# Optimization experiments

Hardware: AMD Instinct MI355X
Metric: run time of the kernel (lower is better)

Reference implementation:

```python
import jax, jax.numpy as jnp
import numpy as np
from functools import partial

NUM_ITERS = 3
NUM_CAPS = 8      # primary capsule count
NUM_CLASSES = 10
OUT_CH = 16       # digit capsule dim
INPUT_SIZE = 32 * 6 * 6  # 1152 primary capsule units per capsule map


def squash(s, axis=-1):
    # faithful to non_linear_squashing: s * (||s||^2/(1+||s||^2)) / (||s||+1e-10)
    norm_sqr = jnp.sum(s * s, axis=axis, keepdims=True)
    scale = jnp.sqrt(norm_sqr) + 1e-10
    mag = norm_sqr / (1.0 + norm_sqr)
    return s * mag / scale


def conv2d(x, w, b, stride):
    y = jax.lax.conv_general_dilated(
        x, w, window_strides=(stride, stride), padding='VALID',
        dimension_numbers=('NCHW', 'OIHW', 'NCHW'))
    return y + b[None, :, None, None]


def setup_inputs() -> dict:
    key = jax.random.key(0)
    ks = jax.random.split(key, 6)
    B = 256
    x = jax.random.normal(ks[0], (B, 1, 28, 28), dtype=jnp.float32)
    conv_w = jax.random.normal(ks[1], (256, 1, 9, 9), dtype=jnp.float32) * 0.05
    conv_b = jax.random.normal(ks[2], (256,), dtype=jnp.float32) * 0.05
    # 8 primary capsule conv units (256->32 each) fused into one 256->256 conv
    prim_w = jax.random.normal(ks[3], (NUM_CAPS * 32, 256, 9, 9), dtype=jnp.float32) * 0.02
    prim_b = jax.random.normal(ks[4], (NUM_CAPS * 32,), dtype=jnp.float32) * 0.02
    # digit routing weights (input_size, num_classes, out_channels, num_capsules)
    digit_w = jax.random.normal(ks[5], (INPUT_SIZE, NUM_CLASSES, OUT_CH, NUM_CAPS), dtype=jnp.float32)
    return {'x': x, 'conv_w': conv_w, 'conv_b': conv_b,
            'prim_w': prim_w, 'prim_b': prim_b, 'digit_w': digit_w}


def reference(x, conv_w, conv_b, prim_w, prim_b, digit_w):
    B = x.shape[0]
    # conv stack: 1->256 k9 s1 + ReLU  (28 -> 20); pool is MaxPool2d(1,1) = identity
    h = jax.nn.relu(conv2d(x, conv_w, conv_b, stride=1))  # (B,256,20,20)
    # primary capsules: 8 convs 256->32 k9 s2, no activation (nl_activation=False)
    p = conv2d(h, prim_w, prim_b, stride=2)               # (B,256,6,6)
    u = p.reshape(B, NUM_CAPS, -1)                        # (B,8,1152)
    u = squash(u, axis=-1)
    # digit layer with dynamic routing
    # u_i: (B, IS, 8);  u_j_i[b,i,c,o] = sum_k W[i,c,o,k] * u_i[b,i,k]
    u_i = jnp.transpose(u, (0, 2, 1))                     # (B,1152,8)
    u_j_i = jnp.einsum('icok,bik->bico', digit_w, u_i)    # (B,1152,10,16)
    b_ij = jnp.zeros((INPUT_SIZE, NUM_CLASSES), dtype=x.dtype)
    out = None
    for _ in range(NUM_ITERS):
        c_ij = jax.nn.softmax(b_ij, axis=0)               # softmax over input capsules (dim=1 in torch)
        s_j = jnp.einsum('ic,bico->bco', c_ij, u_j_i)     # (B,10,16)
        # original squashes (B,1,C,16,1) along dim=2 == the CLASS axis
        out = squash(s_j, axis=1)                         # (B,10,16)
        # agreement: mean over batch of <u_j_i, v_j>
        u_v = jnp.einsum('bico,bco->ic', u_j_i, out) / B  # (1152,10)
        b_ij = b_ij + u_v
    # torch returns out.squeeze(1) with shape (B, C, 16, 1)
    return out[..., None]
```

## Files before the change

### kernel.cpp

```cpp
#include <hip/hip_runtime.h>
#include <cstdint>
#include <cstddef>


typedef __attribute__((ext_vector_type(8))) short short8;
typedef __attribute__((ext_vector_type(4))) float f32x4;

#define PHALF 2359296

__device__ __forceinline__ unsigned short f2bf_rn(float x) {
    unsigned u = __float_as_uint(x);
    unsigned r = (u + 0x7fffu + ((u >> 16) & 1u)) >> 16;
    return (unsigned short)r;
}

__global__ void k_makew(const float* __restrict__ w2,
                        unsigned short* __restrict__ wt) {
    __shared__ float lw[20736];
    int ocg = blockIdx.x, icg = blockIdx.y, t = threadIdx.x;
    for (int idx = t; idx < 20736; idx += 256) {
        int row = idx / 81, k = idx % 81;
        int oc_l = row >> 5, ic_l = row & 31;
        lw[idx] = w2[((size_t)(ocg * 8 + oc_l) * 256 + icg * 32 + ic_l) * 81 + k];
    }
    __syncthreads();
    for (int idx = t; idx < 2592; idx += 256) {
        int k = idx >> 5;
        int r = idx & 31;
        int oc_l = r >> 2, sl = r & 3;
        unsigned short hi8[8];
        #pragma unroll
        for (int j = 0; j < 8; j++)
            hi8[j] = f2bf_rn(lw[(oc_l * 32 + sl * 8 + j) * 81 + k]);
        size_t o = ((size_t)(k * 256 + ocg * 8 + oc_l)) * 256 + icg * 32 + sl * 8;
        *(uint4*)&wt[o] = *(uint4*)hi8;
    }
}

__global__ void k_conv1(const float* __restrict__ x, const float* __restrict__ cw,
                        const float* __restrict__ cb,
                        unsigned short* __restrict__ h) {
    __shared__ float img[784];
    __shared__ float wsm[32 * 81];
    int b = blockIdx.x, ocg = blockIdx.y, t = threadIdx.x;
    for (int idx = t; idx < 784; idx += 256) img[idx] = x[b * 784 + idx];
    for (int idx = t; idx < 2592; idx += 256) wsm[idx] = cw[ocg * 2592 + idx];
    __syncthreads();
    int oc_l = t & 31, g = t >> 5;
    int oc = ocg * 32 + oc_l;
    float bias = cb[oc];
    const float* wp = &wsm[oc_l * 81];
    for (int q = g; q < 100; q += 8) {
        int py = q / 5, qx = (q % 5) * 4;
        float a0 = bias, a1 = bias, a2 = bias, a3 = bias;
        #pragma unroll
        for (int ky = 0; ky < 9; ky++) {
            const float* ir = &img[(py + ky) * 28 + qx];
            float r[12];
            #pragma unroll
            for (int j = 0; j < 12; j++) r[j] = ir[j];
            #pragma unroll
            for (int kx = 0; kx < 9; kx++) {
                float w = wp[ky * 9 + kx];
                a0 += r[kx] * w; a1 += r[kx + 1] * w;
                a2 += r[kx + 2] * w; a3 += r[kx + 3] * w;
            }
        }
        float v[4] = { fmaxf(a0, 0.f), fmaxf(a1, 0.f), fmaxf(a2, 0.f), fmaxf(a3, 0.f) };
        size_t base = ((size_t)b * 400 + py * 20 + qx) * 256 + oc;
        #pragma unroll
        for (int j = 0; j < 4; j++)
            h[base + (size_t)j * 256] = f2bf_rn(v[j]);
    }
}

__global__ __launch_bounds__(256, 4) void k_conv2m(
    const unsigned short* __restrict__ h,
    const unsigned short* __restrict__ wt,
    float* __restrict__ p0, float* __restrict__ p1,
    float* __restrict__ p2, float* __restrict__ p3)
{
    __shared__ unsigned short smem[14336];
    const int t = threadIdx.x;
    const int w = t >> 6, l = t & 63;
    const int mb = blockIdx.x, nb = blockIdx.y, zz = blockIdx.z;
    const int half = zz >> 1, seg = zz & 1;

    const unsigned short* src;
    int nld, sbase;
    unsigned rowbase[8];
    if (w < 2) {
        src = h; nld = 6; sbase = w * 3072;
        #pragma unroll
        for (int ld = 0; ld < 6; ld++) {
            int row = w * 48 + ld * 8 + (l >> 3);
            int c = l & 7;
            int g = c ^ (row & 7);
            int P = mb * 96 + row;
            int b = P / 36, o = P % 36;
            int oy = o / 6, ox = o % 6;
            rowbase[ld] = (unsigned)((b * 400 + oy * 40 + ox * 2) * 256 + half * 128 + g * 8);
        }
    } else {
        src = wt; nld = 8; sbase = 6144 + (w - 2) * 4096;
        #pragma unroll
        for (int ld = 0; ld < 8; ld++) {
            int oc = (w - 2) * 64 + ld * 8 + (l >> 3);
            int c = l & 7;
            int g = c ^ (oc & 7);
            rowbase[ld] = (unsigned)((nb * 128 + oc) * 256 + half * 128 + g * 8);
        }
    }

    const int wm = w & 1, wn = w >> 1;
    const int lane16 = l & 15, q = l >> 4;

    f32x4 acc[3][4] = {};

    const int pos0 = seg ? 41 : 0;
    const int pos1 = seg ? 81 : 41;
    for (int pos = pos0; pos < pos1; ++pos) {
        const int ky = pos / 9, kx = pos - ky * 9;
        const unsigned kbase = (w < 2) ? (unsigned)((ky * 20 + kx) * 256)
                                       : (unsigned)(pos * 65536);
        for (int icc = 0; icc < 2; ++icc) {
            const unsigned kofs = kbase + icc * 64;
            __syncthreads();
            for (int ld = 0; ld < nld; ld++) {
                __builtin_amdgcn_global_load_lds(
                    (const __attribute__((address_space(1))) unsigned int*)(const void*)(src + rowbase[ld] + kofs),
                    (__attribute__((address_space(3))) unsigned int*)(void*)(smem + sbase + ld * 512),
                    16, 0, 0);
            }
            __syncthreads();
            #pragma unroll
            for (int ic2 = 0; ic2 < 2; ic2++) {
                short8 a[3], b[4];
                #pragma unroll
                for (int mt = 0; mt < 3; mt++) {
                    int pixL = wm * 48 + mt * 16 + lane16;
                    int ps = (ic2 * 4 + q) ^ (pixL & 7);
                    a[mt] = *(const short8*)(smem + pixL * 64 + ps * 8);
                }
                #pragma unroll
                for (int nt = 0; nt < 4; nt++) {
                    int ocL = wn * 64 + nt * 16 + lane16;
                    int ps = (ic2 * 4 + q) ^ (ocL & 7);
                    b[nt] = *(const short8*)(smem + 6144 + ocL * 64 + ps * 8);
                }
                #pragma unroll
                for (int mt = 0; mt < 3; mt++)
                    #pragma unroll
                    for (int nt = 0; nt < 4; nt++)
                        acc[mt][nt] = __builtin_amdgcn_mfma_f32_16x16x32_bf16(a[mt], b[nt], acc[mt][nt], 0, 0, 0);
            }
        }
    }

    float* pout = (zz == 0) ? p0 : (zz == 1) ? p1 : (zz == 2) ? p2 : p3;
    #pragma unroll
    for (int mt = 0; mt < 3; mt++) {
        int pixG = mb * 96 + wm * 48 + mt * 16 + q * 4;
        int b = pixG / 36, p36 = pixG % 36;
        #pragma unroll
        for (int nt = 0; nt < 4; nt++) {
            int oc = nb * 128 + wn * 64 + nt * 16 + lane16;
            *(f32x4*)&pout[((size_t)(b * 256 + oc)) * 36 + p36] = acc[mt][nt];
        }
    }
}

__global__ void k_squash1(const float* __restrict__ q0, const float* __restrict__ q1,
                          const float* __restrict__ q2, const float* __restrict__ q3,
                          const float* __restrict__ prim_b, float* __restrict__ U) {
    __shared__ float red[4];
    int b = blockIdx.x >> 3, cap = blockIdx.x & 7;
    int t = threadIdx.x;
    size_t base = ((size_t)b * 256 + cap * 32) * 36;
    const float* pa = q0 + base;
    const float* pb = q1 + base;
    const float* pc = q2 + base;
    const float* pd = q3 + base;
    float v[5];
    float ss = 0.f;
    #pragma unroll
    for (int j = 0; j < 5; j++) {
        int idx = t + j * 256;
        if (idx < 1152) {
            int ch_l = idx / 36;
            float val = pa[idx] + pb[idx] + pc[idx] + pd[idx] + prim_b[cap * 32 + ch_l];
            v[j] = val; ss += val * val;
        } else v[j] = 0.f;
    }
    for (int off = 32; off; off >>= 1) ss += __shfl_down(ss, off);
    if ((t & 63) == 0) red[t >> 6] = ss;
    __syncthreads();
    float n2 = red[0] + red[1] + red[2] + red[3];
    float f = (n2 / (1.0f + n2)) / (sqrtf(n2) + 1e-10f);
    #pragma unroll
    for (int j = 0; j < 5; j++) {
        int idx = t + j * 256;
        if (idx < 1152) U[(size_t)b * 9216 + idx * 8 + cap] = v[j] * f;
    }
}

__global__ void k_dwt2(const float* __restrict__ dw, float* __restrict__ dwT2) {
    int co = blockIdx.x, t = threadIdx.x;
    int c = co >> 4, o = co & 15;
    const float* base = dw + c * 128 + o * 8;
    float* out = dwT2 + (size_t)co * 9216;
    for (int idx = t; idx < 9216; idx += 256) {
        int i = idx >> 3, k = idx & 7;
        out[idx] = base[(size_t)i * 1280 + k];
    }
}

__global__ void k_ut(const float* __restrict__ U, float* __restrict__ UT) {
    __shared__ float tl[64][65];
    int ikb = blockIdx.x, bb = blockIdx.y, t = threadIdx.x;
    for (int idx = t; idx < 1024; idx += 256) {
        int row = idx >> 4, c4 = idx & 15;
        float4 v = *(const float4*)&U[(size_t)(bb * 64 + row) * 9216 + ikb * 64 + c4 * 4];
        tl[c4 * 4 + 0][row] = v.x;
        tl[c4 * 4 + 1][row] = v.y;
        tl[c4 * 4 + 2][row] = v.z;
        tl[c4 * 4 + 3][row] = v.w;
    }
    __syncthreads();
    for (int idx = t; idx < 1024; idx += 256) {
        int row = idx >> 4, c4 = idx & 15;
        float4 v = make_float4(tl[row][c4 * 4 + 0], tl[row][c4 * 4 + 1],
                               tl[row][c4 * 4 + 2], tl[row][c4 * 4 + 3]);
        *(float4*)&UT[(size_t)(ikb * 64 + row) * 256 + bb * 64 + c4 * 4] = v;
    }
}

__global__ void k_softmax(const float* __restrict__ bij, float* __restrict__ csm) {
    __shared__ float red[4];
    int c = blockIdx.x, t = threadIdx.x;
    float vals[5];
    float mx = -1e30f;
    #pragma unroll
    for (int j = 0; j < 5; j++) {
        int i = t + j * 256;
        vals[j] = (i < 1152) ? bij[i * 10 + c] : -1e30f;
        mx = fmaxf(mx, vals[j]);
    }
    for (int off = 32; off; off >>= 1) mx = fmaxf(mx, __shfl_down(mx, off));
    if ((t & 63) == 0) red[t >> 6] = mx;
    __syncthreads();
    mx = fmaxf(fmaxf(red[0], red[1]), fmaxf(red[2], red[3]));
    __syncthreads();
    float s = 0.f;
    #pragma unroll
    for (int j = 0; j < 5; j++) {
        int i = t + j * 256;
        vals[j] = (i < 1152) ? expf(vals[j] - mx) : 0.f;
        s += vals[j];
    }
    for (int off = 32; off; off >>= 1) s += __shfl_down(s, off);
    if ((t & 63) == 0) red[t >> 6] = s;
    __syncthreads();
    s = red[0] + red[1] + red[2] + red[3];
    float inv = 1.0f / s;
    #pragma unroll
    for (int j = 0; j < 5; j++) {
        int i = t + j * 256;
        if (i < 1152) csm[i * 10 + c] = vals[j] * inv;
    }
}

__global__ __launch_bounds__(256) void k_gemm1(const float* __restrict__ U,
                                               const float* __restrict__ dwT2,
                                               const float* __restrict__ csm,
                                               float* __restrict__ part,
                                               int uniform) {
    __shared__ float Us[32 * 36];
    __shared__ float WsT[5120];
    __shared__ float cl[360];
    int mb = blockIdx.x, kc = blockIdx.y, t = threadIdx.x;
    int tc = t & 15, tb = t >> 4;
    if (!uniform)
        for (int idx = t; idx < 360; idx += 256) cl[idx] = csm[kc * 360 + idx];
    const float uscale = 1.0f / 1152.0f;
    float acc[2][10] = {};
    for (int ks = 0; ks < 9; ks++) {
        __syncthreads();
        {
            int bb = t >> 3, k4 = t & 7;
            *(float4*)&Us[bb * 36 + k4 * 4] =
                *(const float4*)&U[(size_t)(mb * 32 + bb) * 9216 + kc * 288 + ks * 32 + k4 * 4];
        }
        #pragma unroll
        for (int pass = 0; pass < 5; pass++) {
            int s = t + pass * 256;
            int co = s >> 3, p = s & 7;
            int kq = p ^ (co & 7);
            int ikl = ks * 32 + kq * 4;
            float4 v = *(const float4*)&dwT2[(size_t)co * 9216 + kc * 288 + ikl];
            float sc = uniform ? uscale : cl[(ikl >> 3) * 10 + (co >> 4)];
            v.x *= sc; v.y *= sc; v.z *= sc; v.w *= sc;
            *(float4*)&WsT[s * 4] = v;
        }
        __syncthreads();
        float a0[32], a1[32];
        #pragma unroll
        for (int kq = 0; kq < 8; kq++) {
            float4 v0 = *(const float4*)&Us[(tb * 2) * 36 + kq * 4];
            float4 v1 = *(const float4*)&Us[(tb * 2 + 1) * 36 + kq * 4];
            a0[kq * 4 + 0] = v0.x; a0[kq * 4 + 1] = v0.y; a0[kq * 4 + 2] = v0.z; a0[kq * 4 + 3] = v0.w;
            a1[kq * 4 + 0] = v1.x; a1[kq * 4 + 1] = v1.y; a1[kq * 4 + 2] = v1.z; a1[kq * 4 + 3] = v1.w;
        }
        #pragma unroll
        for (int j = 0; j < 10; j++) {
            int co = tc + 16 * j;
            int cx = co & 7, cbase = co * 32;
            #pragma unroll
            for (int kq = 0; kq < 8; kq++) {
                float4 wv = *(const float4*)&WsT[cbase + ((kq ^ cx) << 2)];
                acc[0][j] += a0[kq * 4 + 0] * wv.x; acc[0][j] += a0[kq * 4 + 1] * wv.y;
                acc[0][j] += a0[kq * 4 + 2] * wv.z; acc[0][j] += a0[kq * 4 + 3] * wv.w;
                acc[1][j] += a1[kq * 4 + 0] * wv.x; acc[1][j] += a1[kq * 4 + 1] * wv.y;
                acc[1][j] += a1[kq * 4 + 2] * wv.z; acc[1][j] += a1[kq * 4 + 3] * wv.w;
            }
        }
    }
    #pragma unroll
    for (int r = 0; r < 2; r++)
        #pragma unroll
        for (int j = 0; j < 10; j++)
            part[(size_t)kc * 40960 + (mb * 32 + tb * 2 + r) * 160 + tc + 16 * j] = acc[r][j];
}

__global__ void k_redsq(const float* __restrict__ part, float* __restrict__ out,
                        float* __restrict__ outT, int writeT) {
    __shared__ float sl[160];
    __shared__ float n2s[16];
    int b = blockIdx.x, t = threadIdx.x;
    float s = 0.f;
    if (t < 160) {
        for (int kc = 0; kc < 32; kc++) s += part[(size_t)kc * 40960 + b * 160 + t];
        sl[t] = s;
    }
    __syncthreads();
    if (t < 16) {
        float n2 = 0.f;
        #pragma unroll
        for (int c = 0; c < 10; c++) { float v = sl[c * 16 + t]; n2 += v * v; }
        n2s[t] = n2;
    }
    __syncthreads();
    if (t < 160) {
        float n2 = n2s[t & 15];
        float f = (n2 / (1.0f + n2)) / (sqrtf(n2) + 1e-10f);
        float r = s * f;
        out[(size_t)b * 160 + t] = r;
        if (writeT) outT[(size_t)t * 256 + b] = r;
    }
}

__global__ __launch_bounds__(256) void k_g2uv(const float* __restrict__ UT,
                                              const float* __restrict__ outTg,
                                              const float* __restrict__ dw,
                                              float* __restrict__ bij) {
    __shared__ float UsT[1024];
    __shared__ float OsT[5120];
    __shared__ float dwl[5120];
    __shared__ float sb[320];
    int blk = blockIdx.x, t = threadIdx.x;
    int tc = t & 15, tm = t >> 4;
    for (int idx = t; idx < 5120; idx += 256)
        dwl[idx] = dw[(size_t)blk * 5120 + idx];
    float acc[2][10] = {};
    for (int bs = 0; bs < 256; bs += 32) {
        __syncthreads();
        {
            int m = t >> 3, p = t & 7;
            int kq = p ^ (m & 7);
            *(float4*)&UsT[t * 4] =
                *(const float4*)&UT[(size_t)(blk * 32 + m) * 256 + bs + kq * 4];
        }
        #pragma unroll
        for (int pass = 0; pass < 5; pass++) {
            int s = t + pass * 256;
            int co = s >> 3, p = s & 7;
            int kq = p ^ (co & 7);
            *(float4*)&OsT[s * 4] =
                *(const float4*)&outTg[(size_t)co * 256 + bs + kq * 4];
        }
        __syncthreads();
        float a0[32], a1[32];
        int m0 = tm * 2, m1 = tm * 2 + 1;
        #pragma unroll
        for (int kq = 0; kq < 8; kq++) {
            float4 v0 = *(const float4*)&UsT[m0 * 32 + ((kq ^ (m0 & 7)) << 2)];
            float4 v1 = *(const float4*)&UsT[m1 * 32 + ((kq ^ (m1 & 7)) << 2)];
            a0[kq * 4 + 0] = v0.x; a0[kq * 4 + 1] = v0.y; a0[kq * 4 + 2] = v0.z; a0[kq * 4 + 3] = v0.w;
            a1[kq * 4 + 0] = v1.x; a1[kq * 4 + 1] = v1.y; a1[kq * 4 + 2] = v1.z; a1[kq * 4 + 3] = v1.w;
        }
        #pragma unroll
        for (int j = 0; j < 10; j++) {
            int co = tc + 16 * j;
            int cx = co & 7, cbase = co * 32;
            #pragma unroll
            for (int kq = 0; kq < 8; kq++) {
                float4 wv = *(const float4*)&OsT[cbase + ((kq ^ cx) << 2)];
                acc[0][j] += a0[kq * 4 + 0] * wv.x; acc[0][j] += a0[kq * 4 + 1] * wv.y;
                acc[0][j] += a0[kq * 4 + 2] * wv.z; acc[0][j] += a0[kq * 4 + 3] * wv.w;
                acc[1][j] += a1[kq * 4 + 0] * wv.x; acc[1][j] += a1[kq * 4 + 1] * wv.y;
                acc[1][j] += a1[kq * 4 + 2] * wv.z; acc[1][j] += a1[kq * 4 + 3] * wv.w;
            }
        }
    }
    #pragma unroll
    for (int r = 0; r < 2; r++) {
        int ik_l = tm * 2 + r;
        int i_l = ik_l >> 3, k = ik_l & 7;
        #pragma unroll
        for (int j = 0; j < 10; j++) {
            float v = acc[r][j] * dwl[i_l * 1280 + (j * 16 + tc) * 8 + k];
            v += __shfl_down(v, 8, 16);
            v += __shfl_down(v, 4, 16);
            v += __shfl_down(v, 2, 16);
            v += __shfl_down(v, 1, 16);
            if (tc == 0) sb[ik_l * 10 + j] = v;
        }
    }
    __syncthreads();
    if (t < 40) {
        int i_l = t / 10, c = t % 10;
        float s = 0.f;
        #pragma unroll
        for (int kk = 0; kk < 8; kk++) s += sb[(i_l * 8 + kk) * 10 + c];
        size_t o = (size_t)(blk * 4 + i_l) * 10 + c;
        bij[o] += s * (1.0f / 256.0f);
    }
}

extern "C" void kernel_launch(void* const* d_in, const int* in_sizes, int n_in,
                              void* d_out, int out_size, void* d_ws, size_t ws_size,
                              hipStream_t stream) {
    const float* x      = (const float*)d_in[0];
    const float* conv_w = (const float*)d_in[1];
    const float* conv_b = (const float*)d_in[2];
    const float* prim_w = (const float*)d_in[3];
    const float* prim_b = (const float*)d_in[4];
    const float* dw     = (const float*)d_in[5];

    char* wsb = (char*)d_ws;
    unsigned short* h  = (unsigned short*)(wsb);
    unsigned short* wt = (unsigned short*)(wsb + 52428800);
    float* pp0  = (float*)(wsb + 63045632);
    float* pp1  = (float*)(wsb + 72482816);
    float* U    = (float*)(wsb + 81920000);
    float* dwT2 = (float*)(wsb + 91357184);
    float* pp3  = (float*)(wsb + 91357184);
    float* part = (float*)(wsb + 97255424);
    float* csm  = (float*)(wsb + 102498304);
    float* bij  = (float*)(wsb + 102544384);
    float* outT = (float*)(wsb + 102590464);
    float* outw = (float*)(wsb + 102754304);
    float* UT   = (float*)(wsb + 102918144);
    float* pp2  = (float*)(wsb + 102918144);

    k_makew<<<dim3(32, 8), 256, 0, stream>>>(prim_w, wt);
    k_conv1<<<dim3(256, 8), 256, 0, stream>>>(x, conv_w, conv_b, h);
    k_conv2m<<<dim3(96, 2, 4), 256, 0, stream>>>(h, wt, pp0, pp1, pp2, pp3);
    k_squash1<<<2048, 256, 0, stream>>>(pp0, pp1, pp2, pp3, prim_b, U);
    k_dwt2<<<160, 256, 0, stream>>>(dw, dwT2);
    k_ut<<<dim3(144, 4), 256, 0, stream>>>(U, UT);
    hipMemsetAsync(bij, 0, 11520 * sizeof(float), stream);

    k_gemm1<<<dim3(8, 32), 256, 0, stream>>>(U, dwT2, csm, part, 1);
    k_redsq<<<256, 256, 0, stream>>>(part, outw, outT, 1);
    k_g2uv<<<288, 256, 0, stream>>>(UT, outT, dw, bij);
    k_softmax<<<10, 256, 0, stream>>>(bij, csm);
    k_gemm1<<<dim3(8, 32), 256, 0, stream>>>(U, dwT2, csm, part, 0);
    k_redsq<<<256, 256, 0, stream>>>(part, outw, outT, 1);
    k_g2uv<<<288, 256, 0, stream>>>(UT, outT, dw, bij);
    k_softmax<<<10, 256, 0, stream>>>(bij, csm);
    k_gemm1<<<dim3(8, 32), 256, 0, stream>>>(U, dwT2, csm, part, 0);
    k_redsq<<<256, 256, 0, stream>>>(part, (float*)d_out, outT, 0);
}
```

Measured before the change: 490.7 us.

## Double-buffer primary conv LDS staging with 32-channel K steps

Restructures the primary-capsule conv GEMM main loop so it prefetches the next K slice into a second LDS buffer while computing on the current one. Each stage now holds 32 input channels instead of 64, and the XOR swizzle on shared-memory rows is dropped. One barrier per step replaces two and global-to-LDS latency is meant to overlap with MFMA work. The cost is twice as many, smaller steps, and possible LDS bank conflicts without the swizzle.

```diff
diff --git a/kernel.cpp b/kernel.cpp
--- a/kernel.cpp
+++ b/kernel.cpp
@@ -88,27 +88,26 @@
 
     const unsigned short* src;
     int nld, sbase;
-    unsigned rowbase[8];
-    if (w < 2) {
-        src = h; nld = 6; sbase = w * 3072;
-        #pragma unroll
-        for (int ld = 0; ld < 6; ld++) {
-            int row = w * 48 + ld * 8 + (l >> 3);
-            int c = l & 7;
-            int g = c ^ (row & 7);
+    unsigned rowbase[4];
+    const bool isA = (w < 2);
+    if (isA) {
+        src = h; nld = 3; sbase = w * 1536;
+        #pragma unroll
+        for (int ld = 0; ld < 3; ld++) {
+            int row = w * 48 + ld * 16 + (l >> 2);
+            int c = l & 3;
             int P = mb * 96 + row;
             int b = P / 36, o = P % 36;
             int oy = o / 6, ox = o % 6;
-            rowbase[ld] = (unsigned)((b * 400 + oy * 40 + ox * 2) * 256 + half * 128 + g * 8);
+            rowbase[ld] = (unsigned)((b * 400 + oy * 40 + ox * 2) * 256 + half * 128 + c * 8);
         }
     } else {
-        src = wt; nld = 8; sbase = 6144 + (w - 2) * 4096;
-        #pragma unroll
-        for (int ld = 0; ld < 8; ld++) {
-            int oc = (w - 2) * 64 + ld * 8 + (l >> 3);
-            int c = l & 7;
-            int g = c ^ (oc & 7);
-            rowbase[ld] = (unsigned)((nb * 128 + oc) * 256 + half * 128 + g * 8);
+        src = wt; nld = 4; sbase = 3072 + (w - 2) * 2048;
+        #pragma unroll
+        for (int ld = 0; ld < 4; ld++) {
+            int oc = (w - 2) * 64 + ld * 16 + (l >> 2);
+            int c = l & 3;
+            rowbase[ld] = (unsigned)((nb * 128 + oc) * 256 + half * 128 + c * 8);
         }
     }
 
@@ -118,46 +117,56 @@
     f32x4 acc[3][4] = {};
 
     const int pos0 = seg ? 41 : 0;
-    const int pos1 = seg ? 81 : 41;
-    for (int pos = pos0; pos < pos1; ++pos) {
-        const int ky = pos / 9, kx = pos - ky * 9;
-        const unsigned kbase = (w < 2) ? (unsigned)((ky * 20 + kx) * 256)
-                                       : (unsigned)(pos * 65536);
-        for (int icc = 0; icc < 2; ++icc) {
-            const unsigned kofs = kbase + icc * 64;
-            __syncthreads();
-            for (int ld = 0; ld < nld; ld++) {
-                __builtin_amdgcn_global_load_lds(
-                    (const __attribute__((address_space(1))) unsigned int*)(const void*)(src + rowbase[ld] + kofs),
-                    (__attribute__((address_space(3))) unsigned int*)(void*)(smem + sbase + ld * 512),
-                    16, 0, 0);
-            }
-            __syncthreads();
+    const int npos = seg ? 40 : 41;
+    const int NR = npos * 4;
+
+    auto kofs_of = [&](int sr) -> unsigned {
+        int pos = pos0 + (sr >> 2), q32 = sr & 3;
+        if (isA) {
+            int ky = pos / 9, kx = pos - ky * 9;
+            return (unsigned)((ky * 20 + kx) * 256 + q32 * 32);
+        }
+        return (unsigned)(pos * 65536 + q32 * 32);
+    };
+    auto stage = [&](int bf, unsigned kofs) {
+        for (int ld = 0; ld < nld; ld++) {
+            __builtin_amdgcn_global_load_lds(
+                (const __attribute__((address_space(1))) unsigned int*)(const void*)(src + rowbase[ld] + kofs),
+                (__attribute__((address_space(3))) unsigned int*)(void*)(smem + bf * 7168 + sbase + ld * 512),
+                16, 0, 0);
+        }
+    };
+    auto compute = [&](int bf) {
+        const unsigned short* bufp = smem + bf * 7168;
+        short8 a[3], b[4];
+        #pragma unroll
+        for (int mt = 0; mt < 3; mt++) {
+            int pixL = wm * 48 + mt * 16 + lane16;
+            a[mt] = *(const short8*)(bufp + pixL * 32 + q * 8);
+        }
+        #pragma unroll
+        for (int nt = 0; nt < 4; nt++) {
+            int ocL = wn * 64 + nt * 16 + lane16;
+            b[nt] = *(const short8*)(bufp + 3072 + ocL * 32 + q * 8);
+        }
+        #pragma unroll
+        for (int mt = 0; mt < 3; mt++)
             #pragma unroll
-            for (int ic2 = 0; ic2 < 2; ic2++) {
-                short8 a[3], b[4];
-                #pragma unroll
-                for (int mt = 0; mt < 3; mt++) {
-                    int pixL = wm * 48 + mt * 16 + lane16;
-                    int ps = (ic2 * 4 + q) ^ (pixL & 7);
-                    a[mt] = *(const short8*)(smem + pixL * 64 + ps * 8);
-                }
-                #pragma unroll
-                for (int nt = 0; nt < 4; nt++) {
-                    int ocL = wn * 64 + nt * 16 + lane16;
-                    int ps = (ic2 * 4 + q) ^ (ocL & 7);
-                    b[nt] = *(const short8*)(smem + 6144 + ocL * 64 + ps * 8);
-                }
-                #pragma unroll
-                for (int mt = 0; mt < 3; mt++)
-                    #pragma unroll
-                    for (int nt = 0; nt < 4; nt++)
-                        acc[mt][nt] = __builtin_amdgcn_mfma_f32_16x16x32_bf16(a[mt], b[nt], acc[mt][nt], 0, 0, 0);
-            }
-        }
-    }
-
-    float* pout = (zz == 0) ? p0 : (zz == 1) ? p1 : (zz == 2) ? p2 : p3;
+            for (int nt = 0; nt < 4; nt++)
+                acc[mt][nt] = __builtin_amdgcn_mfma_f32_16x16x32_bf16(a[mt], b[nt], acc[mt][nt], 0, 0, 0);
+    };
+
+    stage(0, kofs_of(0));
+    __syncthreads();
+    int cur = 0;
+    for (int sr = 0; sr < NR - 1; ++sr) {
+        stage(cur ^ 1, kofs_of(sr + 1));
+        compute(cur);
+        __syncthreads();
+        cur ^= 1;
+    }
+    compute(cur);
+
     #pragma unroll
     for (int mt = 0; mt < 3; mt++) {
         int pixG = mb * 96 + wm * 48 + mt * 16 + q * 4;
@@ -165,6 +174,7 @@
         #pragma unroll
         for (int nt = 0; nt < 4; nt++) {
             int oc = nb * 128 + wn * 64 + nt * 16 + lane16;
+            float* pout = (zz == 0) ? p0 : (zz == 1) ? p1 : (zz == 2) ? p2 : p3;
             *(f32x4*)&pout[((size_t)(b * 256 + oc)) * 36 + p36] = acc[mt][nt];
         }
     }
```

Measured after the change: 506.7 us. 3.3% more time.

## Merge conv1 and weight prep into one launch, drop U transpose kernel

Applied to the files above, without the earlier changes.

Combines the first convolution and the bf16 weight-repacking kernel into a single launch, so one grid runs both with block ranges split by block index. The weight repack becomes finer grained, with one output channel per block over 2048 blocks. Removes the separate U-transpose kernel; the agreement kernel now reads U directly and transposes into its swizzled shared tile. This saves launches and a round trip of U through memory, but the global reads of U in the agreement kernel are strided and its shared-memory scatter writes may have bank conflicts.

```diff
diff --git a/kernel.cpp b/kernel.cpp
--- a/kernel.cpp
+++ b/kernel.cpp
@@ -14,63 +14,62 @@
     return (unsigned short)r;
 }
 
-__global__ void k_makew(const float* __restrict__ w2,
-                        unsigned short* __restrict__ wt) {
-    __shared__ float lw[20736];
-    int ocg = blockIdx.x, icg = blockIdx.y, t = threadIdx.x;
-    for (int idx = t; idx < 20736; idx += 256) {
-        int row = idx / 81, k = idx % 81;
-        int oc_l = row >> 5, ic_l = row & 31;
-        lw[idx] = w2[((size_t)(ocg * 8 + oc_l) * 256 + icg * 32 + ic_l) * 81 + k];
-    }
-    __syncthreads();
-    for (int idx = t; idx < 2592; idx += 256) {
-        int k = idx >> 5;
-        int r = idx & 31;
-        int oc_l = r >> 2, sl = r & 3;
-        unsigned short hi8[8];
-        #pragma unroll
-        for (int j = 0; j < 8; j++)
-            hi8[j] = f2bf_rn(lw[(oc_l * 32 + sl * 8 + j) * 81 + k]);
-        size_t o = ((size_t)(k * 256 + ocg * 8 + oc_l)) * 256 + icg * 32 + sl * 8;
-        *(uint4*)&wt[o] = *(uint4*)hi8;
-    }
-}
-
-__global__ void k_conv1(const float* __restrict__ x, const float* __restrict__ cw,
-                        const float* __restrict__ cb,
-                        unsigned short* __restrict__ h) {
-    __shared__ float img[784];
-    __shared__ float wsm[32 * 81];
-    int b = blockIdx.x, ocg = blockIdx.y, t = threadIdx.x;
-    for (int idx = t; idx < 784; idx += 256) img[idx] = x[b * 784 + idx];
-    for (int idx = t; idx < 2592; idx += 256) wsm[idx] = cw[ocg * 2592 + idx];
-    __syncthreads();
-    int oc_l = t & 31, g = t >> 5;
-    int oc = ocg * 32 + oc_l;
-    float bias = cb[oc];
-    const float* wp = &wsm[oc_l * 81];
-    for (int q = g; q < 100; q += 8) {
-        int py = q / 5, qx = (q % 5) * 4;
-        float a0 = bias, a1 = bias, a2 = bias, a3 = bias;
-        #pragma unroll
-        for (int ky = 0; ky < 9; ky++) {
-            const float* ir = &img[(py + ky) * 28 + qx];
-            float r[12];
-            #pragma unroll
-            for (int j = 0; j < 12; j++) r[j] = ir[j];
-            #pragma unroll
-            for (int kx = 0; kx < 9; kx++) {
-                float w = wp[ky * 9 + kx];
-                a0 += r[kx] * w; a1 += r[kx + 1] * w;
-                a2 += r[kx + 2] * w; a3 += r[kx + 3] * w;
+__global__ void k_pre(const float* __restrict__ x, const float* __restrict__ cw,
+                      const float* __restrict__ cb, const float* __restrict__ w2,
+                      unsigned short* __restrict__ h, unsigned short* __restrict__ wt) {
+    __shared__ float sh[3376];
+    int blk = blockIdx.x, t = threadIdx.x;
+    if (blk < 2048) {
+        float* img = sh;
+        float* wsm = sh + 784;
+        int b = blk >> 3, ocg = blk & 7;
+        for (int idx = t; idx < 784; idx += 256) img[idx] = x[b * 784 + idx];
+        for (int idx = t; idx < 2592; idx += 256) wsm[idx] = cw[ocg * 2592 + idx];
+        __syncthreads();
+        int oc_l = t & 31, g = t >> 5;
+        int oc = ocg * 32 + oc_l;
+        float bias = cb[oc];
+        const float* wp = &wsm[oc_l * 81];
+        for (int q = g; q < 100; q += 8) {
+            int py = q / 5, qx = (q % 5) * 4;
+            float a0 = bias, a1 = bias, a2 = bias, a3 = bias;
+            #pragma unroll
+            for (int ky = 0; ky < 9; ky++) {
+                const float* ir = &img[(py + ky) * 28 + qx];
+                float r[12];
+                #pragma unroll
+                for (int j = 0; j < 12; j++) r[j] = ir[j];
+                #pragma unroll
+                for (int kx = 0; kx < 9; kx++) {
+                    float w = wp[ky * 9 + kx];
+                    a0 += r[kx] * w; a1 += r[kx + 1] * w;
+                    a2 += r[kx + 2] * w; a3 += r[kx + 3] * w;
+                }
             }
-        }
-        float v[4] = { fmaxf(a0, 0.f), fmaxf(a1, 0.f), fmaxf(a2, 0.f), fmaxf(a3, 0.f) };
-        size_t base = ((size_t)b * 400 + py * 20 + qx) * 256 + oc;
-        #pragma unroll
-        for (int j = 0; j < 4; j++)
-            h[base + (size_t)j * 256] = f2bf_rn(v[j]);
+            float v[4] = { fmaxf(a0, 0.f), fmaxf(a1, 0.f), fmaxf(a2, 0.f), fmaxf(a3, 0.f) };
+            size_t base = ((size_t)b * 400 + py * 20 + qx) * 256 + oc;
+            #pragma unroll
+            for (int j = 0; j < 4; j++)
+                h[base + (size_t)j * 256] = f2bf_rn(v[j]);
+        }
+    } else {
+        int m2 = blk - 2048;
+        int oc = m2 >> 3, icg = m2 & 7;
+        float* lw2 = sh;
+        for (int idx = t; idx < 2592; idx += 256) {
+            int ic_l = idx / 81, k = idx % 81;
+            lw2[idx] = w2[((size_t)oc * 256 + icg * 32 + ic_l) * 81 + k];
+        }
+        __syncthreads();
+        for (int idx = t; idx < 324; idx += 256) {
+            int k = idx >> 2, sl = idx & 3;
+            unsigned short hi8[8];
+            #pragma unroll
+            for (int j = 0; j < 8; j++)
+                hi8[j] = f2bf_rn(lw2[(sl * 8 + j) * 81 + k]);
+            size_t o = ((size_t)(k * 256 + oc)) * 256 + icg * 32 + sl * 8;
+            *(uint4*)&wt[o] = *(uint4*)hi8;
+        }
     }
 }
 
@@ -157,7 +156,6 @@
         }
     }
 
-    float* pout = (zz == 0) ? p0 : (zz == 1) ? p1 : (zz == 2) ? p2 : p3;
     #pragma unroll
     for (int mt = 0; mt < 3; mt++) {
         int pixG = mb * 96 + wm * 48 + mt * 16 + q * 4;
@@ -165,6 +163,7 @@
         #pragma unroll
         for (int nt = 0; nt < 4; nt++) {
             int oc = nb * 128 + wn * 64 + nt * 16 + lane16;
+            float* pout = (zz == 0) ? p0 : (zz == 1) ? p1 : (zz == 2) ? p2 : p3;
             *(f32x4*)&pout[((size_t)(b * 256 + oc)) * 36 + p36] = acc[mt][nt];
         }
     }
@@ -212,26 +211,6 @@
     for (int idx = t; idx < 9216; idx += 256) {
         int i = idx >> 3, k = idx & 7;
         out[idx] = base[(size_t)i * 1280 + k];
-    }
-}
-
-__global__ void k_ut(const float* __restrict__ U, float* __restrict__ UT) {
-    __shared__ float tl[64][65];
-    int ikb = blockIdx.x, bb = blockIdx.y, t = threadIdx.x;
-    for (int idx = t; idx < 1024; idx += 256) {
-        int row = idx >> 4, c4 = idx & 15;
-        float4 v = *(const float4*)&U[(size_t)(bb * 64 + row) * 9216 + ikb * 64 + c4 * 4];
-        tl[c4 * 4 + 0][row] = v.x;
-        tl[c4 * 4 + 1][row] = v.y;
-        tl[c4 * 4 + 2][row] = v.z;
-        tl[c4 * 4 + 3][row] = v.w;
-    }
-    __syncthreads();
-    for (int idx = t; idx < 1024; idx += 256) {
-        int row = idx >> 4, c4 = idx & 15;
-        float4 v = make_float4(tl[row][c4 * 4 + 0], tl[row][c4 * 4 + 1],
-                               tl[row][c4 * 4 + 2], tl[row][c4 * 4 + 3]);
-        *(float4*)&UT[(size_t)(ikb * 64 + row) * 256 + bb * 64 + c4 * 4] = v;
     }
 }
 
@@ -359,7 +338,7 @@
     }
 }
 
-__global__ __launch_bounds__(256) void k_g2uv(const float* __restrict__ UT,
+__global__ __launch_bounds__(256) void k_g2uv(const float* __restrict__ U,
                                               const float* __restrict__ outTg,
                                               const float* __restrict__ dw,
                                               float* __restrict__ bij) {
@@ -375,10 +354,14 @@
     for (int bs = 0; bs < 256; bs += 32) {
         __syncthreads();
         {
-            int m = t >> 3, p = t & 7;
-            int kq = p ^ (m & 7);
-            *(float4*)&UsT[t * 4] =
-                *(const float4*)&UT[(size_t)(blk * 32 + m) * 256 + bs + kq * 4];
+            int r = t >> 3, c4 = t & 7;
+            float4 v = *(const float4*)&U[(size_t)(bs + r) * 9216 + blk * 32 + c4 * 4];
+            int hi = ((r >> 2)) , lo = (r & 3);
+            int m0 = c4 * 4;
+            UsT[(m0 + 0) * 32 + ((hi ^ ((m0 + 0) & 7)) << 2) + lo] = v.x;
+            UsT[(m0 + 1) * 32 + ((hi ^ ((m0 + 1) & 7)) << 2) + lo] = v.y;
+            UsT[(m0 + 2) * 32 + ((hi ^ ((m0 + 2) & 7)) << 2) + lo] = v.z;
+            UsT[(m0 + 3) * 32 + ((hi ^ ((m0 + 3) & 7)) << 2) + lo] = v.w;
         }
         #pragma unroll
         for (int pass = 0; pass < 5; pass++) {
@@ -460,24 +443,21 @@
     float* bij  = (float*)(wsb + 102544384);
     float* outT = (float*)(wsb + 102590464);
     float* outw = (float*)(wsb + 102754304);
-    float* UT   = (float*)(wsb + 102918144);
     float* pp2  = (float*)(wsb + 102918144);
 
-    k_makew<<<dim3(32, 8), 256, 0, stream>>>(prim_w, wt);
-    k_conv1<<<dim3(256, 8), 256, 0, stream>>>(x, conv_w, conv_b, h);
+    k_pre<<<4096, 256, 0, stream>>>(x, conv_w, conv_b, prim_w, h, wt);
     k_conv2m<<<dim3(96, 2, 4), 256, 0, stream>>>(h, wt, pp0, pp1, pp2, pp3);
     k_squash1<<<2048, 256, 0, stream>>>(pp0, pp1, pp2, pp3, prim_b, U);
     k_dwt2<<<160, 256, 0, stream>>>(dw, dwT2);
-    k_ut<<<dim3(144, 4), 256, 0, stream>>>(U, UT);
     hipMemsetAsync(bij, 0, 11520 * sizeof(float), stream);
 
     k_gemm1<<<dim3(8, 32), 256, 0, stream>>>(U, dwT2, csm, part, 1);
     k_redsq<<<256, 256, 0, stream>>>(part, outw, outT, 1);
-    k_g2uv<<<288, 256, 0, stream>>>(UT, outT, dw, bij);
+    k_g2uv<<<288, 256, 0, stream>>>(U, outT, dw, bij);
     k_softmax<<<10, 256, 0, stream>>>(bij, csm);
     k_gemm1<<<dim3(8, 32), 256, 0, stream>>>(U, dwT2, csm, part, 0);
     k_redsq<<<256, 256, 0, stream>>>(part, outw, outT, 1);
-    k_g2uv<<<288, 256, 0, stream>>>(UT, outT, dw, bij);
+    k_g2uv<<<288, 256, 0, stream>>>(U, outT, dw, bij);
     k_softmax<<<10, 256, 0, stream>>>(bij, csm);
     k_gemm1<<<dim3(8, 32), 256, 0, stream>>>(U, dwT2, csm, part, 0);
     k_redsq<<<256, 256, 0, stream>>>(part, (float*)d_out, outT, 0);
```

Measured after the change: 479.0 us. 1.02x faster.
